# Kernel tuning notes

Hardware: AMD Instinct MI355X
Metric: run time of the kernel (lower is better)

The kernel has to match this reference:

```python
import jax, jax.numpy as jnp
import numpy as np

R = 3              # corr_radius
K = 2 * R + 1      # 7x7 support patch
LEVELS = 4         # corr_levels


def _bilinear(fm, xy):
    # fm: (C,H,W); xy: (M,2) pixel coords (x,y).
    # Matches torch grid_sample(align_corners=True, padding_mode='border'):
    # the normalize->denormalize round-trip is the identity, border clamps coords.
    C, H, W = fm.shape
    x = jnp.clip(xy[:, 0], 0.0, W - 1.0)
    y = jnp.clip(xy[:, 1], 0.0, H - 1.0)
    x0 = jnp.floor(x)
    y0 = jnp.floor(y)
    wx = x - x0
    wy = y - y0
    x0i = x0.astype(jnp.int32)
    y0i = y0.astype(jnp.int32)
    x1i = jnp.minimum(x0i + 1, W - 1)
    y1i = jnp.minimum(y0i + 1, H - 1)
    v00 = fm[:, y0i, x0i]
    v01 = fm[:, y0i, x1i]
    v10 = fm[:, y1i, x0i]
    v11 = fm[:, y1i, x1i]
    out = v00 * (1 - wy) * (1 - wx) + v01 * (1 - wy) * wx + v10 * wy * (1 - wx) + v11 * wy * wx
    return out.T  # (M,C)


_bilinear_b = jax.vmap(_bilinear, in_axes=(0, 0))


def _delta():
    # get_support_points: symmetric (2r+1)x(2r+1) integer offset grid around each point
    d = jnp.arange(-R, R + 1, dtype=jnp.float32)
    ox, oy = jnp.meshgrid(d, d, indexing='ij')
    return jnp.stack([ox, oy], -1).reshape(K * K, 2)


def _corr_level(fmaps, track, coords):
    # fmaps: (B,T,C,H,W); track: (B,K*K,N,C); coords: (B,T,N,2) at this level's scale
    B, T, C, H, W = fmaps.shape
    N = coords.shape[2]
    pts = coords.reshape(B * T, N, 1, 2) + _delta()[None, None]          # (BT,N,KK,2)
    feats = _bilinear_b(fmaps.reshape(B * T, C, H, W),
                        pts.reshape(B * T, N * K * K, 2))                # (BT,N*KK,C)
    corr_feat = feats.reshape(B, T, N, K, K, C)
    tf = track.reshape(B, K, K, N, C).transpose(0, 3, 1, 2, 4)           # (B,N,K,K,C)
    return jnp.einsum('btnhwc,bnijc->btnhwij', corr_feat, tf)


def setup_inputs() -> dict:
    key = jax.random.key(0)
    ks = jax.random.split(key, 10)
    B, T, C, N = 1, 16, 128, 256
    H, W = 96, 128
    inp = {}
    for i in range(LEVELS):
        inp['fmaps%d' % i] = jax.random.normal(ks[i], (B, T, C, H >> i, W >> i), jnp.float32)
        inp['track%d' % i] = jax.random.normal(ks[4 + i], (B, K * K, N, C), jnp.float32)
    u = jax.random.uniform(ks[8], (B, T, N, 2), dtype=jnp.float32)
    inp['coords'] = u * jnp.array([W - 1.0, H - 1.0], jnp.float32)
    return inp


def reference(fmaps0, fmaps1, fmaps2, fmaps3, track0, track1, track2, track3, coords):
    fmaps = [fmaps0, fmaps1, fmaps2, fmaps3]
    tracks = [track0, track1, track2, track3]
    vols = [_corr_level(fmaps[i], tracks[i], coords / (2.0 ** i)) for i in range(LEVELS)]
    return jnp.stack(vols, 0)  # (L,B,T,N,K,K,K,K)
```

## Files before the change

### kernel.cpp

```cpp
#include <hip/hip_runtime.h>

#define KK 49
#define CH 128
#define NN 256
#define TT 16

typedef __attribute__((ext_vector_type(8))) short bf16x8;
typedef __attribute__((ext_vector_type(4))) float f32x4;
typedef __attribute__((ext_vector_type(4))) unsigned int u32x4;

__device__ __forceinline__ unsigned int cvt_pk(float a, float b) {
    unsigned int r;
    asm("v_cvt_pk_bf16_f32 %0, %1, %2" : "=v"(r) : "v"(a), "v"(b));
    return r;
}

__global__ __launch_bounds__(256, 8) void corr_mfma_kernel(
    const float* __restrict__ fm0, const float* __restrict__ tk0,
    const float* __restrict__ fm1, const float* __restrict__ tk1,
    const float* __restrict__ fm2, const float* __restrict__ tk2,
    const float* __restrict__ fm3, const float* __restrict__ tk3,
    const float* __restrict__ coords, float* __restrict__ out)
{
    const int lvl = blockIdx.y;
    const float* fm  = lvl == 0 ? fm0 : lvl == 1 ? fm1 : lvl == 2 ? fm2 : fm3;
    const float* trk = lvl == 0 ? tk0 : lvl == 1 ? tk1 : lvl == 2 ? tk2 : tk3;
    const int H = 96 >> lvl, W = 128 >> lvl;
    const float inv = 1.0f / (float)(1 << lvl);

    __shared__ unsigned int smemPD[64 * 68];
    __shared__ int   rowoff[KK];
    __shared__ float wxs[KK], wys[KK];

    const int tid  = threadIdx.x;
    const int wave = tid >> 6;
    const int lane = tid & 63;
    const int t = blockIdx.x >> 8;
    const int n = blockIdx.x & 255;

    const int mr = lane & 15;
    const int q  = lane >> 4;

    const int ij = min(wave * 16 + mr, KK - 1);
    const float* tb = trk + (size_t)ij * (NN * CH) + (size_t)n * CH + q * 8;
    f32x4 bl[4], bh[4];
    #pragma unroll
    for (int ks = 0; ks < 4; ++ks) {
        bl[ks] = *(const f32x4*)(tb + ks * 32);
        bh[ks] = *(const f32x4*)(tb + ks * 32 + 4);
    }

    const float2 c2 = *(const float2*)(coords + (size_t)(t * NN + n) * 2);
    const float cx = c2.x * inv;
    const float cy = c2.y * inv;
    const int gx0 = (int)floorf(cx) - 3;
    const int gy0 = (int)floorf(cy) - 3;

    if (tid < KK) {
        const int h = tid / 7;
        const int w = tid - h * 7;
        float x = fminf(fmaxf(cx + (float)(h - 3), 0.0f), (float)(W - 1));
        float y = fminf(fmaxf(cy + (float)(w - 3), 0.0f), (float)(H - 1));
        const float x0 = floorf(x), y0 = floorf(y);
        wxs[tid] = x - x0;
        wys[tid] = y - y0;
        const int ix = min(max((int)x0 - gx0, 0), 6);
        const int iy = min(max((int)y0 - gy0, 0), 6);
        rowoff[tid] = (iy * 8 + ix) * 68;
    }

    bf16x8 bfrag[4];
    #pragma unroll
    for (int ks = 0; ks < 4; ++ks) {
        union { bf16x8 v; u32x4 u; } bu;
        bu.u[0] = cvt_pk(bl[ks][0], bl[ks][1]);
        bu.u[1] = cvt_pk(bl[ks][2], bl[ks][3]);
        bu.u[2] = cvt_pk(bh[ks][0], bh[ks][1]);
        bu.u[3] = cvt_pk(bh[ks][2], bh[ks][3]);
        bfrag[ks] = bu.v;
    }

    {
        const int HW = H * W;
        const int py = min(max(gy0 + (lane >> 3), 0), H - 1);
        const int px = min(max(gx0 + (lane & 7), 0), W - 1);
        const float* base = fm + (size_t)t * CH * HW + (py * W + px);
        const int j0 = wave * 16;
        #pragma unroll
        for (int c4 = 0; c4 < 4; ++c4) {
            const int jb = j0 + c4 * 4;
            float a[8];
            #pragma unroll
            for (int i = 0; i < 8; ++i)
                a[i] = base[(size_t)(2 * jb + i) * HW];
            u32x4 wv;
            wv[0] = cvt_pk(a[0], a[1]);
            wv[1] = cvt_pk(a[2], a[3]);
            wv[2] = cvt_pk(a[4], a[5]);
            wv[3] = cvt_pk(a[6], a[7]);
            *(u32x4*)&smemPD[lane * 68 + jb] = wv;
        }
    }
    __syncthreads();

    f32x4 acc[4];
    #pragma unroll
    for (int m = 0; m < 4; ++m) acc[m] = (f32x4){0.f, 0.f, 0.f, 0.f};
    {
        const unsigned short* P = (const unsigned short*)smemPD;
        #pragma unroll
        for (int ks = 0; ks < 4; ++ks) {
            const int kof = ks * 32 + q * 8;
            #pragma unroll
            for (int m = 0; m < 4; ++m) {
                const bf16x8 a = *(const bf16x8*)&P[(m * 16 + mr) * 136 + kof];
                acc[m] = __builtin_amdgcn_mfma_f32_16x16x32_bf16(a, bfrag[ks], acc[m], 0, 0, 0);
            }
        }
    }
    __syncthreads();

    {
        float* D = (float*)smemPD;
        const int col = wave * 16 + mr;
        #pragma unroll
        for (int m = 0; m < 4; ++m) {
            #pragma unroll
            for (int r = 0; r < 4; ++r) {
                D[(m * 16 + q * 4 + r) * 68 + col] = acc[m][r];
            }
        }
    }
    __syncthreads();

    {
        const float* D = (const float*)smemPD;
        float* op = out + (((size_t)lvl * TT + t) * NN + n) * (KK * KK);
        for (int idx = tid; idx < KK * KK; idx += 256) {
            const int p   = idx / KK;
            const int ijc = idx - p * KK;
            const float wx = wxs[p], wy = wys[p];
            const float* d0 = &D[rowoff[p] + ijc];
            const float v00 = d0[0];
            const float v01 = d0[68];
            const float v10 = d0[8 * 68];
            const float v11 = d0[9 * 68];
            op[idx] = v00 * (1.f - wy) * (1.f - wx) + v01 * (1.f - wy) * wx
                    + v10 * wy * (1.f - wx)       + v11 * wy * wx;
        }
    }
}

extern "C" void kernel_launch(void* const* d_in, const int* in_sizes, int n_in,
                              void* d_out, int out_size, void* d_ws, size_t ws_size,
                              hipStream_t stream) {
    hipLaunchKernelGGL(corr_mfma_kernel, dim3(TT * NN, 4), dim3(256), 0, stream,
                       (const float*)d_in[0], (const float*)d_in[1],
                       (const float*)d_in[2], (const float*)d_in[3],
                       (const float*)d_in[4], (const float*)d_in[5],
                       (const float*)d_in[6], (const float*)d_in[7],
                       (const float*)d_in[8], (float*)d_out);
}
```

Baseline: 387.2 us.

## Vectorize feature-patch gather and transpose shared-memory patch layout

When the 8-wide patch window lies inside the image, each thread issues 16-byte row loads covering 12 consecutive pixels for two channels, selects the 8 needed by shifting, and packs them to bf16 pairs. This replaces scalar, strided per-pixel channel loads. The shared-memory layout is transposed to channel-pair-major (64 channel-pairs by 64 pixels), and the MFMA A-fragments are now assembled from four scalar LDS reads instead of one vector read. Border patches fall back to a scalar gather, which adds a divergent branch and some extra LDS read instructions.

```diff
diff --git a/kernel.cpp b/kernel.cpp
--- a/kernel.cpp
+++ b/kernel.cpp
@@ -4,6 +4,7 @@
 #define CH 128
 #define NN 256
 #define TT 16
+#define PITCH 68
 
 typedef __attribute__((ext_vector_type(8))) short bf16x8;
 typedef __attribute__((ext_vector_type(4))) float f32x4;
@@ -28,7 +29,7 @@
     const int H = 96 >> lvl, W = 128 >> lvl;
     const float inv = 1.0f / (float)(1 << lvl);
 
-    __shared__ unsigned int smemPD[64 * 68];
+    __shared__ unsigned int smemPD[64 * PITCH];
     __shared__ int   rowoff[KK];
     __shared__ float wxs[KK], wys[KK];
 
@@ -66,7 +67,7 @@
         wys[tid] = y - y0;
         const int ix = min(max((int)x0 - gx0, 0), 6);
         const int iy = min(max((int)y0 - gy0, 0), 6);
-        rowoff[tid] = (iy * 8 + ix) * 68;
+        rowoff[tid] = (iy * 8 + ix) * PITCH;
     }
 
     bf16x8 bfrag[4];
@@ -82,23 +83,56 @@
 
     {
         const int HW = H * W;
-        const int py = min(max(gy0 + (lane >> 3), 0), H - 1);
-        const int px = min(max(gx0 + (lane & 7), 0), W - 1);
-        const float* base = fm + (size_t)t * CH * HW + (py * W + px);
-        const int j0 = wave * 16;
-        #pragma unroll
-        for (int c4 = 0; c4 < 4; ++c4) {
-            const int jb = j0 + c4 * 4;
-            float a[8];
+        const float* fmt = fm + (size_t)t * CH * HW;
+        const int xal = gx0 & ~3;
+        if (xal >= 0 && xal + 11 <= W - 1) {
+            const int s  = gx0 & 3;
+            const int jj = tid >> 2;
+            const int c0 = 2 * jj;
+            const int r0 = (tid & 3) * 2;
             #pragma unroll
-            for (int i = 0; i < 8; ++i)
-                a[i] = base[(size_t)(2 * jb + i) * HW];
-            u32x4 wv;
-            wv[0] = cvt_pk(a[0], a[1]);
-            wv[1] = cvt_pk(a[2], a[3]);
-            wv[2] = cvt_pk(a[4], a[5]);
-            wv[3] = cvt_pk(a[6], a[7]);
-            *(u32x4*)&smemPD[lane * 68 + jb] = wv;
+            for (int rr = 0; rr < 2; ++rr) {
+                const int r  = r0 + rr;
+                const int py = min(max(gy0 + r, 0), H - 1);
+                const float* rp0 = fmt + (size_t)c0 * HW + (size_t)py * W + xal;
+                const float* rp1 = rp0 + HW;
+                union { f32x4 v[3]; float f[12]; } A, B;
+                A.v[0] = *(const f32x4*)(rp0);
+                A.v[1] = *(const f32x4*)(rp0 + 4);
+                A.v[2] = *(const f32x4*)(rp0 + 8);
+                B.v[0] = *(const f32x4*)(rp1);
+                B.v[1] = *(const f32x4*)(rp1 + 4);
+                B.v[2] = *(const f32x4*)(rp1 + 8);
+                u32x4 w0, w1;
+#define PACKCASE(S) \
+                w0[0] = cvt_pk(A.f[S+0], B.f[S+0]); \
+                w0[1] = cvt_pk(A.f[S+1], B.f[S+1]); \
+                w0[2] = cvt_pk(A.f[S+2], B.f[S+2]); \
+                w0[3] = cvt_pk(A.f[S+3], B.f[S+3]); \
+                w1[0] = cvt_pk(A.f[S+4], B.f[S+4]); \
+                w1[1] = cvt_pk(A.f[S+5], B.f[S+5]); \
+                w1[2] = cvt_pk(A.f[S+6], B.f[S+6]); \
+                w1[3] = cvt_pk(A.f[S+7], B.f[S+7]); break;
+                switch (s) {
+                    case 0:  PACKCASE(0)
+                    case 1:  PACKCASE(1)
+                    case 2:  PACKCASE(2)
+                    default: PACKCASE(3)
+                }
+#undef PACKCASE
+                *(u32x4*)&smemPD[jj * PITCH + r * 8]     = w0;
+                *(u32x4*)&smemPD[jj * PITCH + r * 8 + 4] = w1;
+            }
+        } else {
+            const int py = min(max(gy0 + (lane >> 3), 0), H - 1);
+            const int px = min(max(gx0 + (lane & 7), 0), W - 1);
+            const float* base = fmt + (size_t)py * W + px;
+            #pragma unroll 4
+            for (int jb = wave * 16; jb < wave * 16 + 16; ++jb) {
+                const float a0 = base[(size_t)(2 * jb) * HW];
+                const float a1 = base[(size_t)(2 * jb + 1) * HW];
+                smemPD[jb * PITCH + lane] = cvt_pk(a0, a1);
+            }
         }
     }
     __syncthreads();
@@ -107,14 +141,18 @@
     #pragma unroll
     for (int m = 0; m < 4; ++m) acc[m] = (f32x4){0.f, 0.f, 0.f, 0.f};
     {
-        const unsigned short* P = (const unsigned short*)smemPD;
         #pragma unroll
         for (int ks = 0; ks < 4; ++ks) {
-            const int kof = ks * 32 + q * 8;
+            const int jb = ks * 16 + q * 4;
             #pragma unroll
             for (int m = 0; m < 4; ++m) {
-                const bf16x8 a = *(const bf16x8*)&P[(m * 16 + mr) * 136 + kof];
-                acc[m] = __builtin_amdgcn_mfma_f32_16x16x32_bf16(a, bfrag[ks], acc[m], 0, 0, 0);
+                const int g = m * 16 + mr;
+                union { bf16x8 v; unsigned int u[4]; } au;
+                au.u[0] = smemPD[(jb + 0) * PITCH + g];
+                au.u[1] = smemPD[(jb + 1) * PITCH + g];
+                au.u[2] = smemPD[(jb + 2) * PITCH + g];
+                au.u[3] = smemPD[(jb + 3) * PITCH + g];
+                acc[m] = __builtin_amdgcn_mfma_f32_16x16x32_bf16(au.v, bfrag[ks], acc[m], 0, 0, 0);
             }
         }
     }
@@ -127,7 +165,7 @@
         for (int m = 0; m < 4; ++m) {
             #pragma unroll
             for (int r = 0; r < 4; ++r) {
-                D[(m * 16 + q * 4 + r) * 68 + col] = acc[m][r];
+                D[(m * 16 + q * 4 + r) * PITCH + col] = acc[m][r];
             }
         }
     }
@@ -142,9 +180,9 @@
             const float wx = wxs[p], wy = wys[p];
             const float* d0 = &D[rowoff[p] + ijc];
             const float v00 = d0[0];
-            const float v01 = d0[68];
-            const float v10 = d0[8 * 68];
-            const float v11 = d0[9 * 68];
+            const float v01 = d0[PITCH];
+            const float v10 = d0[8 * PITCH];
+            const float v11 = d0[9 * PITCH];
             op[idx] = v00 * (1.f - wy) * (1.f - wx) + v01 * (1.f - wy) * wx
                     + v10 * wy * (1.f - wx)       + v11 * wy * wx;
         }
```

New measurement: 419.4 us. +8.3%, slower.

## Prepack feature maps and tracks to channel-last bf16 in workspace, load via LDS DMA

Applied to the files above, without the earlier changes.

Adds two prepass kernels that convert the feature maps to a channel-last bf16 layout and the track features to bf16 in the workspace. The main kernel then gathers the 8x8 pixel patch with global_load_lds into an XOR-swizzled shared-memory tile, replacing the old strided per-channel fp32 gathers and in-kernel conversion. This trades two extra launches and a full pass over the inputs for contiguous 16-byte gathers in the main kernel. The original kernel is kept as a fallback when the workspace is too small.

```diff
diff --git a/kernel.cpp b/kernel.cpp
--- a/kernel.cpp
+++ b/kernel.cpp
@@ -4,6 +4,15 @@
 #define CH 128
 #define NN 256
 #define TT 16
+#define PITCH 68
+
+#define FMB0_OFF 0u
+#define FMB1_OFF 12582912u
+#define FMB2_OFF 15728640u
+#define FMB3_OFF 16515072u
+#define TKB_OFF  16711680u
+#define TK_WORDS 802816u
+#define WS_NEEDED 79691776ull
 
 typedef __attribute__((ext_vector_type(8))) short bf16x8;
 typedef __attribute__((ext_vector_type(4))) float f32x4;
@@ -15,7 +24,180 @@
     return r;
 }
 
-__global__ __launch_bounds__(256, 8) void corr_mfma_kernel(
+__global__ void fm_prepass(
+    const float* __restrict__ fm0, const float* __restrict__ fm1,
+    const float* __restrict__ fm2, const float* __restrict__ fm3,
+    unsigned int* __restrict__ ws)
+{
+    const int lvl = blockIdx.y;
+    const float* fm = lvl == 0 ? fm0 : lvl == 1 ? fm1 : lvl == 2 ? fm2 : fm3;
+    unsigned int* dstl = ws + (lvl == 0 ? FMB0_OFF : lvl == 1 ? FMB1_OFF :
+                               lvl == 2 ? FMB2_OFF : FMB3_OFF);
+    const int H = 96 >> lvl, W = 128 >> lvl;
+    const int bx = blockIdx.x;
+    if (bx >= TT * H) return;
+    const int t = bx / H;
+    const int y = bx - t * H;
+    const int tid = threadIdx.x;
+
+    const float* src = fm + ((size_t)t * CH * H + y) * W;
+    unsigned int* dst = dstl + ((size_t)(t * H + y) * W) * 64;
+
+    __shared__ unsigned int Tt[16 * 68];
+
+    const int ntile = W >> 4;
+    for (int xt = 0; xt < ntile; ++xt) {
+        #pragma unroll
+        for (int it = 0; it < 4; ++it) {
+            const int cp = it * 16 + (tid >> 4);
+            const int x  = tid & 15;
+            const float f0 = src[(size_t)(2 * cp)     * H * W + xt * 16 + x];
+            const float f1 = src[(size_t)(2 * cp + 1) * H * W + xt * 16 + x];
+            Tt[x * 68 + cp] = cvt_pk(f0, f1);
+        }
+        __syncthreads();
+        {
+            const int x = tid >> 4, ct = tid & 15;
+            const u32x4 v = *(const u32x4*)&Tt[x * 68 + ct * 4];
+            *(u32x4*)&dst[(size_t)(xt * 16 + x) * 64 + ct * 4] = v;
+        }
+        __syncthreads();
+    }
+}
+
+__global__ void tk_prepass(
+    const float* __restrict__ tk0, const float* __restrict__ tk1,
+    const float* __restrict__ tk2, const float* __restrict__ tk3,
+    unsigned int* __restrict__ ws)
+{
+    const int lvl = blockIdx.y;
+    const float* src = lvl == 0 ? tk0 : lvl == 1 ? tk1 : lvl == 2 ? tk2 : tk3;
+    const unsigned int idx = blockIdx.x * 256 + threadIdx.x;
+    const float2 v = ((const float2*)src)[idx];
+    ws[TKB_OFF + (size_t)lvl * TK_WORDS + idx] = cvt_pk(v.x, v.y);
+}
+
+__global__ __launch_bounds__(256, 8) void corr_mfma_v5(
+    const unsigned int* __restrict__ ws,
+    const float* __restrict__ coords, float* __restrict__ out)
+{
+    const int lvl = blockIdx.y;
+    const unsigned int* fmb = ws + (lvl == 0 ? FMB0_OFF : lvl == 1 ? FMB1_OFF :
+                                    lvl == 2 ? FMB2_OFF : FMB3_OFF);
+    const unsigned int* tkb = ws + TKB_OFF + (size_t)lvl * TK_WORDS;
+    const int H = 96 >> lvl, W = 128 >> lvl;
+    const float inv = 1.0f / (float)(1 << lvl);
+
+    __shared__ unsigned int smemPD[64 * PITCH];
+    __shared__ int   rowoff[KK];
+    __shared__ float wxs[KK], wys[KK];
+
+    const int tid  = threadIdx.x;
+    const int wave = tid >> 6;
+    const int lane = tid & 63;
+    const int t = blockIdx.x >> 8;
+    const int n = blockIdx.x & 255;
+    const int mr = lane & 15;
+    const int q  = lane >> 4;
+
+    const int ij = min(wave * 16 + mr, KK - 1);
+    const unsigned int* tb = tkb + ((size_t)(ij * NN + n) << 6) + (q << 2);
+    u32x4 braw[4];
+    #pragma unroll
+    for (int ks = 0; ks < 4; ++ks) braw[ks] = *(const u32x4*)(tb + (ks << 4));
+
+    const float2 c2 = *(const float2*)(coords + (size_t)(t * NN + n) * 2);
+    const float cx = c2.x * inv;
+    const float cy = c2.y * inv;
+    const int gx0 = (int)floorf(cx) - 3;
+    const int gy0 = (int)floorf(cy) - 3;
+
+    if (tid < KK) {
+        const int h = tid / 7;
+        const int w = tid - h * 7;
+        float x = fminf(fmaxf(cx + (float)(h - 3), 0.0f), (float)(W - 1));
+        float y = fminf(fmaxf(cy + (float)(w - 3), 0.0f), (float)(H - 1));
+        const float x0 = floorf(x), y0 = floorf(y);
+        wxs[tid] = x - x0;
+        wys[tid] = y - y0;
+        const int ix = min(max((int)x0 - gx0, 0), 6);
+        const int iy = min(max((int)y0 - gy0, 0), 6);
+        rowoff[tid] = (iy * 8 + ix) * PITCH;
+    }
+
+    {
+        const unsigned int* fmt = fmb + (size_t)t * (H * W * 64);
+        #pragma unroll
+        for (int it = 0; it < 4; ++it) {
+            const int g  = wave * 16 + it * 4 + (lane >> 4);
+            const int py = min(max(gy0 + (g >> 3), 0), H - 1);
+            const int px = min(max(gx0 + (g & 7), 0), W - 1);
+            const int c4 = lane & 15;
+            const unsigned int* src = fmt + ((size_t)(py * W + px) << 6)
+                                          + ((c4 ^ (g & 7)) << 2);
+            unsigned int* dst = &smemPD[(wave * 16 + it * 4) << 6];
+            __builtin_amdgcn_global_load_lds(
+                (const __attribute__((address_space(1))) unsigned int*)src,
+                (__attribute__((address_space(3))) unsigned int*)dst, 16, 0, 0);
+        }
+    }
+    __syncthreads();
+
+    f32x4 acc[4];
+    #pragma unroll
+    for (int m = 0; m < 4; ++m) acc[m] = (f32x4){0.f, 0.f, 0.f, 0.f};
+    {
+        #pragma unroll
+        for (int ks = 0; ks < 4; ++ks) {
+            union { bf16x8 v; u32x4 u; } bu; bu.u = braw[ks];
+            #pragma unroll
+            for (int m = 0; m < 4; ++m) {
+                const int g = m * 16 + mr;
+                union { bf16x8 v; u32x4 u; } au;
+                au.u = *(const u32x4*)&smemPD[(g << 6) + ((((ks << 2) + q) ^ (g & 7)) << 2)];
+                acc[m] = __builtin_amdgcn_mfma_f32_16x16x32_bf16(au.v, bu.v, acc[m], 0, 0, 0);
+            }
+        }
+    }
+    __syncthreads();
+
+    {
+        float* D = (float*)smemPD;
+        const int col = wave * 16 + mr;
+        #pragma unroll
+        for (int m = 0; m < 4; ++m) {
+            #pragma unroll
+            for (int r = 0; r < 4; ++r) {
+                D[(m * 16 + q * 4 + r) * PITCH + col] = acc[m][r];
+            }
+        }
+    }
+    __syncthreads();
+
+    {
+        const float* D = (const float*)smemPD;
+        float* op = out + (((size_t)lvl * TT + t) * NN + n) * (KK * KK);
+        for (int idx = tid; idx < KK * KK; idx += 256) {
+            const int p   = idx / KK;
+            const int ijc = idx - p * KK;
+            const float wx = wxs[p], wy = wys[p];
+            const float* d0 = &D[rowoff[p] + ijc];
+            const float v00 = d0[0];
+            const float v01 = d0[PITCH];
+            const float v10 = d0[8 * PITCH];
+            const float v11 = d0[9 * PITCH];
+            op[idx] = v00 * (1.f - wy) * (1.f - wx) + v01 * (1.f - wy) * wx
+                    + v10 * wy * (1.f - wx)       + v11 * wy * wx;
+        }
+    }
+}
+
+__device__ __forceinline__ unsigned int f2bf(float f) {
+    unsigned int u = __float_as_uint(f);
+    return (u + 0x7fffu + ((u >> 16) & 1u)) >> 16;
+}
+
+__global__ __launch_bounds__(256, 8) void corr_mfma_fallback(
     const float* __restrict__ fm0, const float* __restrict__ tk0,
     const float* __restrict__ fm1, const float* __restrict__ tk1,
     const float* __restrict__ fm2, const float* __restrict__ tk2,
@@ -28,7 +210,7 @@
     const int H = 96 >> lvl, W = 128 >> lvl;
     const float inv = 1.0f / (float)(1 << lvl);
 
-    __shared__ unsigned int smemPD[64 * 68];
+    __shared__ unsigned int smemPD[64 * PITCH];
     __shared__ int   rowoff[KK];
     __shared__ float wxs[KK], wys[KK];
 
@@ -37,7 +219,6 @@
     const int lane = tid & 63;
     const int t = blockIdx.x >> 8;
     const int n = blockIdx.x & 255;
-
     const int mr = lane & 15;
     const int q  = lane >> 4;
 
@@ -66,7 +247,7 @@
         wys[tid] = y - y0;
         const int ix = min(max((int)x0 - gx0, 0), 6);
         const int iy = min(max((int)y0 - gy0, 0), 6);
-        rowoff[tid] = (iy * 8 + ix) * 68;
+        rowoff[tid] = (iy * 8 + ix) * PITCH;
     }
 
     bf16x8 bfrag[4];
@@ -84,7 +265,7 @@
         const int HW = H * W;
         const int py = min(max(gy0 + (lane >> 3), 0), H - 1);
         const int px = min(max(gx0 + (lane & 7), 0), W - 1);
-        const float* base = fm + (size_t)t * CH * HW + (py * W + px);
+        const float* base = fm + (size_t)t * CH * HW + (size_t)py * W + px;
         const int j0 = wave * 16;
         #pragma unroll
         for (int c4 = 0; c4 < 4; ++c4) {
@@ -98,7 +279,7 @@
             wv[1] = cvt_pk(a[2], a[3]);
             wv[2] = cvt_pk(a[4], a[5]);
             wv[3] = cvt_pk(a[6], a[7]);
-            *(u32x4*)&smemPD[lane * 68 + jb] = wv;
+            *(u32x4*)&smemPD[lane * PITCH + jb] = wv;
         }
     }
     __syncthreads();
@@ -127,7 +308,7 @@
         for (int m = 0; m < 4; ++m) {
             #pragma unroll
             for (int r = 0; r < 4; ++r) {
-                D[(m * 16 + q * 4 + r) * 68 + col] = acc[m][r];
+                D[(m * 16 + q * 4 + r) * PITCH + col] = acc[m][r];
             }
         }
     }
@@ -142,9 +323,9 @@
             const float wx = wxs[p], wy = wys[p];
             const float* d0 = &D[rowoff[p] + ijc];
             const float v00 = d0[0];
-            const float v01 = d0[68];
-            const float v10 = d0[8 * 68];
-            const float v11 = d0[9 * 68];
+            const float v01 = d0[PITCH];
+            const float v10 = d0[8 * PITCH];
+            const float v11 = d0[9 * PITCH];
             op[idx] = v00 * (1.f - wy) * (1.f - wx) + v01 * (1.f - wy) * wx
                     + v10 * wy * (1.f - wx)       + v11 * wy * wx;
         }
@@ -154,10 +335,22 @@
 extern "C" void kernel_launch(void* const* d_in, const int* in_sizes, int n_in,
                               void* d_out, int out_size, void* d_ws, size_t ws_size,
                               hipStream_t stream) {
-    hipLaunchKernelGGL(corr_mfma_kernel, dim3(TT * NN, 4), dim3(256), 0, stream,
-                       (const float*)d_in[0], (const float*)d_in[1],
-                       (const float*)d_in[2], (const float*)d_in[3],
-                       (const float*)d_in[4], (const float*)d_in[5],
-                       (const float*)d_in[6], (const float*)d_in[7],
-                       (const float*)d_in[8], (float*)d_out);
-}
+    if (ws_size < WS_NEEDED || d_ws == nullptr) {
+        hipLaunchKernelGGL(corr_mfma_fallback, dim3(TT * NN, 4), dim3(256), 0, stream,
+                           (const float*)d_in[0], (const float*)d_in[1],
+                           (const float*)d_in[2], (const float*)d_in[3],
+                           (const float*)d_in[4], (const float*)d_in[5],
+                           (const float*)d_in[6], (const float*)d_in[7],
+                           (const float*)d_in[8], (float*)d_out);
+        return;
+    }
+    unsigned int* ws = (unsigned int*)d_ws;
+    hipLaunchKernelGGL(fm_prepass, dim3(TT * 96, 4), dim3(256), 0, stream,
+                       (const float*)d_in[0], (const float*)d_in[2],
+                       (const float*)d_in[4], (const float*)d_in[6], ws);
+    hipLaunchKernelGGL(tk_prepass, dim3(TK_WORDS / 256, 4), dim3(256), 0, stream,
+                       (const float*)d_in[1], (const float*)d_in[3],
+                       (const float*)d_in[5], (const float*)d_in[7], ws);
+    hipLaunchKernelGGL(corr_mfma_v5, dim3(TT * NN, 4), dim3(256), 0, stream,
+                       (const unsigned int*)ws, (const float*)d_in[8], (float*)d_out);
+}
```

New measurement: 338.4 us. 12.6% less time.
